# Performance work log

Hardware: AMD Instinct MI355X
Metric: run time of the kernel (lower is better)

The kernel has to match this reference:

```python
import jax, jax.numpy as jnp
import numpy as np

H = 16          # num heads
HD = 88         # head dim = 1408 / 16
IMG = 336
PATCH = 14
THETA = 10000.0
IDX = IMG // PATCH          # 24 patches per side
SEQ = IDX * IDX + 1         # 576 patches + 1 CLS slot = 577


def _vision_rope_cos_sin():
    # Faithful to HF Llama4VisionRotaryEmbedding (rope_type='llama4', complex64):
    # 2D rope over (x, y) patch coordinates; CLS token gets zero rotation.
    img_idx = np.arange(IDX * IDX, dtype=np.int64).reshape(-1, 1)
    img_idx = np.concatenate([img_idx, img_idx[:1]], axis=0)
    img_idx[-1, -1] = -2  # CLS token marker
    fx = img_idx % IDX
    fy = img_idx // IDX
    freq_dim = HD // 2  # 44
    rope_freq = 1.0 / (THETA ** (np.arange(0, freq_dim, 2)[: freq_dim // 2].astype(np.float64) / freq_dim))
    freqs_x = np.repeat((fx + 1)[..., None] * rope_freq[None, None, :], 2, axis=-1)
    freqs_y = np.repeat((fy + 1)[..., None] * rope_freq[None, None, :], 2, axis=-1)
    freqs = np.concatenate([freqs_x, freqs_y], axis=-1)[..., ::2]  # [SEQ, 1, HD//2]
    freqs = np.where(img_idx.reshape(-1, 1, 1) < 0, 0.0, freqs)
    return jnp.asarray(np.cos(freqs), jnp.float32), jnp.asarray(np.sin(freqs), jnp.float32)


def _apply_rope(x, cos, sin):
    # x: [B, S, H, HD]; treat last dim as HD//2 complex pairs, rotate by e^{i*freq}
    xr = x.reshape(*x.shape[:-1], HD // 2, 2)
    a, b = xr[..., 0], xr[..., 1]               # [B, S, H, HD//2]
    out_r = a * cos - b * sin                   # cos/sin [S,1,HD//2] broadcast over B,H
    out_i = a * sin + b * cos
    return jnp.stack([out_r, out_i], axis=-1).reshape(x.shape)


def setup_inputs() -> dict:
    key = jax.random.key(0)
    ks = jax.random.split(key, 9)
    D = H * HD  # 1408
    B, S = 32, SEQ
    s = 0.02
    return {
        "hidden_states": jax.random.normal(ks[0], (B, S, D), jnp.float32),
        "wq": jax.random.normal(ks[1], (D, D), jnp.float32) * s,
        "bq": jax.random.normal(ks[2], (D,), jnp.float32) * s,
        "wk": jax.random.normal(ks[3], (D, D), jnp.float32) * s,
        "bk": jax.random.normal(ks[4], (D,), jnp.float32) * s,
        "wv": jax.random.normal(ks[5], (D, D), jnp.float32) * s,
        "bv": jax.random.normal(ks[6], (D,), jnp.float32) * s,
        "wo": jax.random.normal(ks[7], (D, D), jnp.float32) * s,
        "bo": jax.random.normal(ks[8], (D,), jnp.float32) * s,
    }


def reference(hidden_states, wq, bq, wk, bk, wv, bv, wo, bo):
    B, S, D = hidden_states.shape
    cos, sin = _vision_rope_cos_sin()
    # QKV projections (torch Linear convention: y = x @ W.T + b)
    q = (hidden_states @ wq.T + bq).reshape(B, S, H, HD)
    k = (hidden_states @ wk.T + bk).reshape(B, S, H, HD)
    v = (hidden_states @ wv.T + bv).reshape(B, S, H, HD)
    q = _apply_rope(q, cos, sin)
    k = _apply_rope(k, cos, sin)
    # Full (non-causal) self-attention
    scores = jnp.einsum('bqhd,bkhd->bhqk', q, k) * (HD ** -0.5)
    probs = jax.nn.softmax(scores, axis=-1)
    attn = jnp.einsum('bhqk,bkhd->bqhd', probs, v).reshape(B, S, D)
    return attn @ wo.T + bo
```

## Files before the change

kernel.cpp:

```cpp
#include <hip/hip_runtime.h>
#include <hip/hip_bf16.h>
#include <cstdint>
#include <cstddef>

#define NHEADS 16
#define HDIM   88
#define SEQLEN 577
#define NBATCH 32
#define DMODEL 1408
#define MROWS  (NBATCH * SEQLEN)
#define MTILES 145
#define MPAD   (MTILES * 128)
#define SP     592
#define DP     96
#define NFREQ  44
#define NBH    (NBATCH * NHEADS)

typedef __attribute__((ext_vector_type(8))) short short8;
typedef __attribute__((ext_vector_type(4))) float floatx4;

__device__ __forceinline__ unsigned short f2bf(float f) {
    union { float f; unsigned u; } v; v.f = f;
    unsigned u = v.u;
    u += 0x7fffu + ((u >> 16) & 1u);
    return (unsigned short)(u >> 16);
}

__device__ __forceinline__ void gload_lds16(const void* g, void* lds) {
    __builtin_amdgcn_global_load_lds(
        (__attribute__((address_space(1))) unsigned int*)(void*)(g ? (void*)g : (void*)g),
        (__attribute__((address_space(3))) unsigned int*)lds, 16, 0, 0);
}

__global__ void l4v_rope_table(float* __restrict__ cos_t, float* __restrict__ sin_t) {
    int idx = blockIdx.x * blockDim.x + threadIdx.x;
    if (idx >= SEQLEN * NFREQ) return;
    int s = idx / NFREQ, j = idx % NFREQ;
    float ang = 0.0f;
    if (s != SEQLEN - 1) {
        int coord = (j < 22) ? (s % 24) : (s / 24);
        int i = (j < 22) ? j : j - 22;
        float rf = __expf(-(2.0f * (float)i / 44.0f) * 9.21034037197618f);
        ang = (float)(coord + 1) * rf;
    }
    cos_t[idx] = cosf(ang);
    sin_t[idx] = sinf(ang);
}

__global__ void l4v_cvt_bf16(const float* __restrict__ in, unsigned short* __restrict__ out, int n) {
    int i = (blockIdx.x * blockDim.x + threadIdx.x) * 4;
    if (i + 3 < n) {
        float4 f = *(const float4*)(in + i);
        ushort4 o;
        o.x = f2bf(f.x); o.y = f2bf(f.y); o.z = f2bf(f.z); o.w = f2bf(f.w);
        *(ushort4*)(out + i) = o;
    } else {
        for (; i < n; i++) out[i] = f2bf(in[i]);
    }
}

__global__ __launch_bounds__(256, 2)
void l4v_gemm128(const unsigned short* __restrict__ A,
                 const unsigned short* __restrict__ Bw,
                 const float* __restrict__ bias,
                 const float* __restrict__ cos_t,
                 const float* __restrict__ sin_t,
                 unsigned short* __restrict__ out_bf,
                 float* __restrict__ out_f32,
                 int mode)
{
    __shared__ __align__(16) unsigned short a_sm[128 * 32];
    __shared__ __align__(16) unsigned short b_sm[128 * 32];

    const int tid  = threadIdx.x;
    const int lane = tid & 63;
    const int w    = tid >> 6;
    const int quad = lane >> 4;
    const int c    = lane & 15;
    const int wr   = w >> 1;
    const int wc   = w & 1;
    const int m0   = blockIdx.y * 128;
    const int n0   = blockIdx.x * 128;

    floatx4 acc[4][4];
#pragma unroll
    for (int i = 0; i < 4; i++)
#pragma unroll
        for (int j = 0; j < 4; j++) acc[i][j] = (floatx4)0.0f;

    const int chunk0 = w * 128 + lane;
    const int chunk1 = w * 128 + 64 + lane;
    const int r0 = chunk0 >> 2, ch0 = chunk0 & 3;
    const int r1 = chunk1 >> 2, ch1 = chunk1 & 3;
    const unsigned short* Ab = A  + (size_t)m0 * DMODEL;
    const unsigned short* Bb = Bw + (size_t)n0 * DMODEL;

    for (int k0 = 0; k0 < DMODEL; k0 += 32) {
        gload_lds16(Ab + (size_t)r0 * DMODEL + k0 + ch0 * 8, a_sm + (w * 128) * 8);
        gload_lds16(Ab + (size_t)r1 * DMODEL + k0 + ch1 * 8, a_sm + (w * 128 + 64) * 8);
        gload_lds16(Bb + (size_t)r0 * DMODEL + k0 + ch0 * 8, b_sm + (w * 128) * 8);
        gload_lds16(Bb + (size_t)r1 * DMODEL + k0 + ch1 * 8, b_sm + (w * 128 + 64) * 8);
        __syncthreads();
        short8 af[4], bfr[4];
#pragma unroll
        for (int mt = 0; mt < 4; mt++)
            af[mt] = *(const short8*)(a_sm + (wr * 64 + mt * 16 + c) * 32 + quad * 8);
#pragma unroll
        for (int nt = 0; nt < 4; nt++)
            bfr[nt] = *(const short8*)(b_sm + (wc * 64 + nt * 16 + c) * 32 + quad * 8);
#pragma unroll
        for (int mt = 0; mt < 4; mt++)
#pragma unroll
            for (int nt = 0; nt < 4; nt++)
                acc[mt][nt] = __builtin_amdgcn_mfma_f32_16x16x32_bf16(af[mt], bfr[nt], acc[mt][nt], 0, 0, 0);
        __syncthreads();
    }

    if (mode == 3) {
#pragma unroll
        for (int mt = 0; mt < 4; mt++) {
            int mbase = m0 + wr * 64 + mt * 16 + quad * 4;
#pragma unroll
            for (int nt = 0; nt < 4; nt++) {
                int n = n0 + wc * 64 + nt * 16 + c;
                float bi = bias[n];
#pragma unroll
                for (int r = 0; r < 4; r++) {
                    int m = mbase + r;
                    if (m < MROWS) out_f32[(size_t)m * DMODEL + n] = acc[mt][nt][r] + bi;
                }
            }
        }
        return;
    }

    const bool rope = (mode < 2);
#pragma unroll
    for (int mt = 0; mt < 4; mt++) {
        int mbase = m0 + wr * 64 + mt * 16 + quad * 4;
#pragma unroll
        for (int nt = 0; nt < 4; nt++) {
            int n = n0 + wc * 64 + nt * 16 + c;
            float bi = bias[n];
            int h = n / HDIM, d = n % HDIM, j = d >> 1;
#pragma unroll
            for (int r = 0; r < 4; r++) {
                int m = mbase + r;
                int s = m % SEQLEN;
                int b = m / SEQLEN;
                float v = acc[mt][nt][r] + bi;
                float outv = v;
                if (rope) {
                    float pv = __shfl_xor(v, 1);
                    float cs = cos_t[s * NFREQ + j];
                    float sn = sin_t[s * NFREQ + j];
                    outv = ((d & 1) == 0) ? (v * cs - pv * sn) : (pv * sn + v * cs);
                }
                if (m < MROWS)
                    out_bf[((size_t)(b * NHEADS + h) * SP + s) * DP + d] = f2bf(outv);
            }
        }
    }
}

__global__ __launch_bounds__(256, 2)
void l4v_attn(const unsigned short* __restrict__ Q,
              const unsigned short* __restrict__ K,
              const unsigned short* __restrict__ V,
              unsigned short* __restrict__ Obuf)
{
    __shared__ __align__(16) unsigned short k_sm[64 * DP];
    __shared__ __align__(16) unsigned short v_sm[64 * DP];
    __shared__ __align__(16) unsigned short p_sm[4][16 * 64];

    const int tid  = threadIdx.x;
    const int lane = tid & 63;
    const int w    = tid >> 6;
    const int quad = lane >> 4;
    const int c    = lane & 15;
    const int qt   = blockIdx.x;
    const int bh   = blockIdx.y;
    const size_t base = (size_t)bh * SP * DP;

    short8 aq[3];
    {
        int qrow = qt * 64 + w * 16 + c;
        if (qrow > SP - 1) qrow = SP - 1;
#pragma unroll
        for (int ks = 0; ks < 3; ks++)
            aq[ks] = *(const short8*)(Q + base + (size_t)qrow * DP + ks * 32 + quad * 8);
    }

    float m_run[4], l_run[4];
    floatx4 o_acc[6];
#pragma unroll
    for (int r = 0; r < 4; r++) { m_run[r] = -INFINITY; l_run[r] = 0.0f; }
#pragma unroll
    for (int i = 0; i < 6; i++) o_acc[i] = (floatx4)0.0f;

    const float sl2e = 0.10660035817780522f * 1.4426950408889634f;

    for (int kt = 0; kt < 10; kt++) {
#pragma unroll
        for (int i = 0; i < 3; i++) {
            int chnk = w * 192 + i * 64 + lane;
            int row = chnk / 12, ch = chnk % 12;
            int krow = kt * 64 + row;
            if (krow > SP - 1) krow = SP - 1;
            gload_lds16(K + base + (size_t)krow * DP + ch * 8, k_sm + (w * 192 + i * 64) * 8);
            gload_lds16(V + base + (size_t)krow * DP + ch * 8, v_sm + (w * 192 + i * 64) * 8);
        }
        __syncthreads();

        floatx4 sc[4];
#pragma unroll
        for (int nt = 0; nt < 4; nt++) {
            sc[nt] = (floatx4)0.0f;
#pragma unroll
            for (int ks = 0; ks < 3; ks++) {
                short8 bk = *(const short8*)(k_sm + (nt * 16 + c) * DP + ks * 32 + quad * 8);
                sc[nt] = __builtin_amdgcn_mfma_f32_16x16x32_bf16(aq[ks], bk, sc[nt], 0, 0, 0);
            }
        }

        float t[4][4];
#pragma unroll
        for (int nt = 0; nt < 4; nt++) {
            int skcol = kt * 64 + nt * 16 + c;
            bool valid = (skcol < SEQLEN);
#pragma unroll
            for (int r = 0; r < 4; r++)
                t[nt][r] = valid ? sc[nt][r] * sl2e : -INFINITY;
        }

        float mnew[4], alpha[4];
#pragma unroll
        for (int r = 0; r < 4; r++) {
            float v = fmaxf(fmaxf(t[0][r], t[1][r]), fmaxf(t[2][r], t[3][r]));
#pragma unroll
            for (int off = 1; off < 16; off <<= 1) v = fmaxf(v, __shfl_xor(v, off));
            mnew[r] = fmaxf(m_run[r], v);
            alpha[r] = exp2f(m_run[r] - mnew[r]);
            m_run[r] = mnew[r];
        }

        float p[4][4];
#pragma unroll
        for (int nt = 0; nt < 4; nt++)
#pragma unroll
            for (int r = 0; r < 4; r++)
                p[nt][r] = exp2f(t[nt][r] - mnew[r]);

#pragma unroll
        for (int r = 0; r < 4; r++) {
            float sm = p[0][r] + p[1][r] + p[2][r] + p[3][r];
#pragma unroll
            for (int off = 1; off < 16; off <<= 1) sm += __shfl_xor(sm, off);
            l_run[r] = l_run[r] * alpha[r] + sm;
        }

#pragma unroll
        for (int nt = 0; nt < 4; nt++)
#pragma unroll
            for (int r = 0; r < 4; r++)
                p_sm[w][(quad * 4 + r) * 64 + nt * 16 + c] = f2bf(p[nt][r]);

#pragma unroll
        for (int i = 0; i < 6; i++)
#pragma unroll
            for (int r = 0; r < 4; r++)
                o_acc[i][r] *= alpha[r];

#pragma unroll
        for (int kp = 0; kp < 2; kp++) {
            short8 ap = *(const short8*)(&p_sm[w][c * 64 + kp * 32 + quad * 8]);
#pragma unroll
            for (int d2 = 0; d2 < 6; d2++) {
                short8 bv;
#pragma unroll
                for (int j = 0; j < 8; j++)
                    bv[j] = (short)v_sm[(kp * 32 + quad * 8 + j) * DP + d2 * 16 + c];
                o_acc[d2] = __builtin_amdgcn_mfma_f32_16x16x32_bf16(ap, bv, o_acc[d2], 0, 0, 0);
            }
        }
        __syncthreads();
    }

    const int b = bh >> 4, h = bh & 15;
#pragma unroll
    for (int r = 0; r < 4; r++) {
        int sq = qt * 64 + w * 16 + quad * 4 + r;
        float il = 1.0f / l_run[r];
        if (sq < SEQLEN) {
            size_t rowoff = ((size_t)b * SEQLEN + sq) * DMODEL + h * HDIM;
#pragma unroll
            for (int d2 = 0; d2 < 6; d2++) {
                int d = d2 * 16 + c;
                if (d < HDIM) Obuf[rowoff + d] = f2bf(o_acc[d2][r] * il);
            }
        }
    }
}

extern "C" void kernel_launch(void* const* d_in, const int* in_sizes, int n_in,
                              void* d_out, int out_size, void* d_ws, size_t ws_size,
                              hipStream_t stream)
{
    const float* hs = (const float*)d_in[0];
    const float* wq = (const float*)d_in[1];
    const float* bq = (const float*)d_in[2];
    const float* wk = (const float*)d_in[3];
    const float* bk = (const float*)d_in[4];
    const float* wv = (const float*)d_in[5];
    const float* bv = (const float*)d_in[6];
    const float* wo = (const float*)d_in[7];
    const float* bo = (const float*)d_in[8];
    float* out = (float*)d_out;

    char* ws = (char*)d_ws;
    size_t off = 0;
    auto alloc = [&](size_t bytes) -> char* {
        char* p = ws + off;
        off += (bytes + 255) & ~(size_t)255;
        return p;
    };

    unsigned short* hs_bf = (unsigned short*)alloc((size_t)MPAD * DMODEL * 2);
    unsigned short* wq_bf = (unsigned short*)alloc((size_t)DMODEL * DMODEL * 2);
    unsigned short* wk_bf = (unsigned short*)alloc((size_t)DMODEL * DMODEL * 2);
    unsigned short* wv_bf = (unsigned short*)alloc((size_t)DMODEL * DMODEL * 2);
    unsigned short* wo_bf = (unsigned short*)alloc((size_t)DMODEL * DMODEL * 2);
    unsigned short* qb    = (unsigned short*)alloc((size_t)NBH * SP * DP * 2);
    unsigned short* kb    = (unsigned short*)alloc((size_t)NBH * SP * DP * 2);
    unsigned short* vb    = (unsigned short*)alloc((size_t)NBH * SP * DP * 2);
    float* cos_t = (float*)alloc((size_t)SEQLEN * NFREQ * 4);
    float* sin_t = (float*)alloc((size_t)SEQLEN * NFREQ * 4);
    unsigned short* attn_bf = hs_bf;

    if (off > ws_size) return;

    l4v_rope_table<<<dim3((SEQLEN * NFREQ + 255) / 256), dim3(256), 0, stream>>>(cos_t, sin_t);

    const int nhs = MROWS * DMODEL;
    l4v_cvt_bf16<<<dim3(nhs / 4 / 256), dim3(256), 0, stream>>>(hs, hs_bf, nhs);
    const int nw = DMODEL * DMODEL;
    l4v_cvt_bf16<<<dim3(nw / 4 / 256), dim3(256), 0, stream>>>(wq, wq_bf, nw);
    l4v_cvt_bf16<<<dim3(nw / 4 / 256), dim3(256), 0, stream>>>(wk, wk_bf, nw);
    l4v_cvt_bf16<<<dim3(nw / 4 / 256), dim3(256), 0, stream>>>(wv, wv_bf, nw);
    l4v_cvt_bf16<<<dim3(nw / 4 / 256), dim3(256), 0, stream>>>(wo, wo_bf, nw);

    dim3 ggrid(DMODEL / 128, MTILES);
    l4v_gemm128<<<ggrid, dim3(256), 0, stream>>>(hs_bf, wq_bf, bq, cos_t, sin_t, qb, nullptr, 0);
    l4v_gemm128<<<ggrid, dim3(256), 0, stream>>>(hs_bf, wk_bf, bk, cos_t, sin_t, kb, nullptr, 1);
    l4v_gemm128<<<ggrid, dim3(256), 0, stream>>>(hs_bf, wv_bf, bv, cos_t, sin_t, vb, nullptr, 2);

    l4v_attn<<<dim3(10, NBH), dim3(256), 0, stream>>>(qb, kb, vb, attn_bf);

    l4v_gemm128<<<ggrid, dim3(256), 0, stream>>>(attn_bf, wo_bf, bo, cos_t, sin_t, nullptr, out, 3);
}
```

Before: 1.008 ms.

## Transpose V layout, fuse QKV GEMMs, pad attention LDS and batch query tiles

The GEMM epilogue now writes V in a transposed [bh, d, s] layout. The attention P·V step can then read V fragments with vector LDS loads instead of eight scalar gathers per fragment. The three QKV projections are merged into one launch that picks the weight by blockIdx, and the LDS strides for K, V and P are padded to cut bank conflicts. Each attention block now handles five query tiles with higher launch bounds. In exchange, the V stores in the GEMM become strided 2-byte scatters, K and V are staged through registers instead of direct-to-LDS loads, and the attention grid has fewer blocks.

```diff
diff --git a/kernel.cpp b/kernel.cpp
--- a/kernel.cpp
+++ b/kernel.cpp
@@ -12,6 +12,7 @@
 #define MTILES 145
 #define MPAD   (MTILES * 128)
 #define SP     592
+#define SPT    592
 #define DP     96
 #define NFREQ  44
 #define NBH    (NBATCH * NHEADS)
@@ -28,7 +29,7 @@
 
 __device__ __forceinline__ void gload_lds16(const void* g, void* lds) {
     __builtin_amdgcn_global_load_lds(
-        (__attribute__((address_space(1))) unsigned int*)(void*)(g ? (void*)g : (void*)g),
+        (__attribute__((address_space(1))) unsigned int*)g,
         (__attribute__((address_space(3))) unsigned int*)lds, 16, 0, 0);
 }
 
@@ -59,15 +60,125 @@
     }
 }
 
-__global__ __launch_bounds__(256, 2)
-void l4v_gemm128(const unsigned short* __restrict__ A,
-                 const unsigned short* __restrict__ Bw,
-                 const float* __restrict__ bias,
-                 const float* __restrict__ cos_t,
-                 const float* __restrict__ sin_t,
-                 unsigned short* __restrict__ out_bf,
-                 float* __restrict__ out_f32,
-                 int mode)
+__global__ __launch_bounds__(256, 3)
+void l4v_gemm_qkv(const unsigned short* __restrict__ A,
+                  const unsigned short* __restrict__ Wq,
+                  const unsigned short* __restrict__ Wk,
+                  const unsigned short* __restrict__ Wv,
+                  const float* __restrict__ Bq,
+                  const float* __restrict__ Bk,
+                  const float* __restrict__ Bv,
+                  const float* __restrict__ cos_t,
+                  const float* __restrict__ sin_t,
+                  unsigned short* __restrict__ Oq,
+                  unsigned short* __restrict__ Ok,
+                  unsigned short* __restrict__ OvT)
+{
+    __shared__ __align__(16) unsigned short a_sm[128 * 32];
+    __shared__ __align__(16) unsigned short b_sm[128 * 32];
+
+    const int tid  = threadIdx.x;
+    const int lane = tid & 63;
+    const int w    = tid >> 6;
+    const int quad = lane >> 4;
+    const int c    = lane & 15;
+    const int wr   = w >> 1;
+    const int wc   = w & 1;
+    const int sel  = blockIdx.x % 3;
+    const int n0   = (blockIdx.x / 3) * 128;
+    const int m0   = blockIdx.y * 128;
+
+    const unsigned short* Bw = (sel == 0) ? Wq : (sel == 1) ? Wk : Wv;
+    const float* bias        = (sel == 0) ? Bq : (sel == 1) ? Bk : Bv;
+
+    floatx4 acc[4][4];
+#pragma unroll
+    for (int i = 0; i < 4; i++)
+#pragma unroll
+        for (int j = 0; j < 4; j++) acc[i][j] = (floatx4)0.0f;
+
+    const int chunk0 = w * 128 + lane;
+    const int chunk1 = w * 128 + 64 + lane;
+    const int r0 = chunk0 >> 2, ch0 = chunk0 & 3;
+    const int r1 = chunk1 >> 2, ch1 = chunk1 & 3;
+    const unsigned short* Ab = A  + (size_t)m0 * DMODEL;
+    const unsigned short* Bb = Bw + (size_t)n0 * DMODEL;
+
+    for (int k0 = 0; k0 < DMODEL; k0 += 32) {
+        gload_lds16(Ab + (size_t)r0 * DMODEL + k0 + ch0 * 8, a_sm + (w * 128) * 8);
+        gload_lds16(Ab + (size_t)r1 * DMODEL + k0 + ch1 * 8, a_sm + (w * 128 + 64) * 8);
+        gload_lds16(Bb + (size_t)r0 * DMODEL + k0 + ch0 * 8, b_sm + (w * 128) * 8);
+        gload_lds16(Bb + (size_t)r1 * DMODEL + k0 + ch1 * 8, b_sm + (w * 128 + 64) * 8);
+        __syncthreads();
+        short8 af[4], bfr[4];
+#pragma unroll
+        for (int mt = 0; mt < 4; mt++)
+            af[mt] = *(const short8*)(a_sm + (wr * 64 + mt * 16 + c) * 32 + quad * 8);
+#pragma unroll
+        for (int nt = 0; nt < 4; nt++)
+            bfr[nt] = *(const short8*)(b_sm + (wc * 64 + nt * 16 + c) * 32 + quad * 8);
+#pragma unroll
+        for (int mt = 0; mt < 4; mt++)
+#pragma unroll
+            for (int nt = 0; nt < 4; nt++)
+                acc[mt][nt] = __builtin_amdgcn_mfma_f32_16x16x32_bf16(af[mt], bfr[nt], acc[mt][nt], 0, 0, 0);
+        __syncthreads();
+    }
+
+    if (sel < 2) {
+        unsigned short* outp = (sel == 0) ? Oq : Ok;
+#pragma unroll
+        for (int mt = 0; mt < 4; mt++) {
+            int mbase = m0 + wr * 64 + mt * 16 + quad * 4;
+#pragma unroll
+            for (int nt = 0; nt < 4; nt++) {
+                int n = n0 + wc * 64 + nt * 16 + c;
+                float bi = bias[n];
+                int h = n / HDIM, d = n % HDIM, j = d >> 1;
+#pragma unroll
+                for (int r = 0; r < 4; r++) {
+                    int m = mbase + r;
+                    int b = m / SEQLEN;
+                    int s = m - b * SEQLEN;
+                    float v = acc[mt][nt][r] + bi;
+                    float pv = __shfl_xor(v, 1);
+                    float cs = cos_t[s * NFREQ + j];
+                    float sn = sin_t[s * NFREQ + j];
+                    float outv = ((d & 1) == 0) ? (v * cs - pv * sn) : (pv * sn + v * cs);
+                    if (m < MROWS)
+                        outp[((size_t)(b * NHEADS + h) * SP + s) * DP + d] = f2bf(outv);
+                }
+            }
+        }
+    } else {
+#pragma unroll
+        for (int mt = 0; mt < 4; mt++) {
+            int mbase = m0 + wr * 64 + mt * 16 + quad * 4;
+#pragma unroll
+            for (int nt = 0; nt < 4; nt++) {
+                int n = n0 + wc * 64 + nt * 16 + c;
+                float bi = bias[n];
+                int h = n / HDIM, d = n % HDIM;
+#pragma unroll
+                for (int r = 0; r < 4; r++) {
+                    int m = mbase + r;
+                    if (m < MROWS) {
+                        int b = m / SEQLEN;
+                        int s = m - b * SEQLEN;
+                        OvT[((size_t)((b * NHEADS + h) * DP + d)) * SPT + s] =
+                            f2bf(acc[mt][nt][r] + bi);
+                    }
+                }
+            }
+        }
+    }
+}
+
+__global__ __launch_bounds__(256, 3)
+void l4v_gemm_out(const unsigned short* __restrict__ A,
+                  const unsigned short* __restrict__ Bw,
+                  const float* __restrict__ bias,
+                  float* __restrict__ out_f32)
 {
     __shared__ __align__(16) unsigned short a_sm[128 * 32];
     __shared__ __align__(16) unsigned short b_sm[128 * 32];
@@ -116,25 +227,6 @@
         __syncthreads();
     }
 
-    if (mode == 3) {
-#pragma unroll
-        for (int mt = 0; mt < 4; mt++) {
-            int mbase = m0 + wr * 64 + mt * 16 + quad * 4;
-#pragma unroll
-            for (int nt = 0; nt < 4; nt++) {
-                int n = n0 + wc * 64 + nt * 16 + c;
-                float bi = bias[n];
-#pragma unroll
-                for (int r = 0; r < 4; r++) {
-                    int m = mbase + r;
-                    if (m < MROWS) out_f32[(size_t)m * DMODEL + n] = acc[mt][nt][r] + bi;
-                }
-            }
-        }
-        return;
-    }
-
-    const bool rope = (mode < 2);
 #pragma unroll
     for (int mt = 0; mt < 4; mt++) {
         int mbase = m0 + wr * 64 + mt * 16 + quad * 4;
@@ -142,161 +234,153 @@
         for (int nt = 0; nt < 4; nt++) {
             int n = n0 + wc * 64 + nt * 16 + c;
             float bi = bias[n];
-            int h = n / HDIM, d = n % HDIM, j = d >> 1;
 #pragma unroll
             for (int r = 0; r < 4; r++) {
                 int m = mbase + r;
-                int s = m % SEQLEN;
-                int b = m / SEQLEN;
-                float v = acc[mt][nt][r] + bi;
-                float outv = v;
-                if (rope) {
-                    float pv = __shfl_xor(v, 1);
-                    float cs = cos_t[s * NFREQ + j];
-                    float sn = sin_t[s * NFREQ + j];
-                    outv = ((d & 1) == 0) ? (v * cs - pv * sn) : (pv * sn + v * cs);
-                }
-                if (m < MROWS)
-                    out_bf[((size_t)(b * NHEADS + h) * SP + s) * DP + d] = f2bf(outv);
+                if (m < MROWS) out_f32[(size_t)m * DMODEL + n] = acc[mt][nt][r] + bi;
             }
         }
     }
 }
 
-__global__ __launch_bounds__(256, 2)
+__global__ __launch_bounds__(256, 4)
 void l4v_attn(const unsigned short* __restrict__ Q,
               const unsigned short* __restrict__ K,
-              const unsigned short* __restrict__ V,
+              const unsigned short* __restrict__ VT,
               unsigned short* __restrict__ Obuf)
 {
-    __shared__ __align__(16) unsigned short k_sm[64 * DP];
-    __shared__ __align__(16) unsigned short v_sm[64 * DP];
-    __shared__ __align__(16) unsigned short p_sm[4][16 * 64];
+    __shared__ __align__(16) unsigned short k_sm[64 * 104];
+    __shared__ __align__(16) unsigned short v_sm[96 * 72];
+    __shared__ __align__(16) unsigned short p_sm[4][16 * 72];
 
     const int tid  = threadIdx.x;
     const int lane = tid & 63;
     const int w    = tid >> 6;
     const int quad = lane >> 4;
     const int c    = lane & 15;
-    const int qt   = blockIdx.x;
     const int bh   = blockIdx.y;
-    const size_t base = (size_t)bh * SP * DP;
-
-    short8 aq[3];
-    {
+    const int b    = bh >> 4, h = bh & 15;
+    const size_t base  = (size_t)bh * SP * DP;
+    const size_t baseT = (size_t)bh * DP * SPT;
+    const float sl2e = 0.10660035817780522f * 1.4426950408889634f;
+
+    for (int qi = 0; qi < 5; qi++) {
+        const int qt = blockIdx.x * 5 + qi;
+
         int qrow = qt * 64 + w * 16 + c;
         if (qrow > SP - 1) qrow = SP - 1;
+        short8 aq[3];
 #pragma unroll
         for (int ks = 0; ks < 3; ks++)
             aq[ks] = *(const short8*)(Q + base + (size_t)qrow * DP + ks * 32 + quad * 8);
-    }
-
-    float m_run[4], l_run[4];
-    floatx4 o_acc[6];
-#pragma unroll
-    for (int r = 0; r < 4; r++) { m_run[r] = -INFINITY; l_run[r] = 0.0f; }
-#pragma unroll
-    for (int i = 0; i < 6; i++) o_acc[i] = (floatx4)0.0f;
-
-    const float sl2e = 0.10660035817780522f * 1.4426950408889634f;
-
-    for (int kt = 0; kt < 10; kt++) {
-#pragma unroll
-        for (int i = 0; i < 3; i++) {
-            int chnk = w * 192 + i * 64 + lane;
-            int row = chnk / 12, ch = chnk % 12;
-            int krow = kt * 64 + row;
-            if (krow > SP - 1) krow = SP - 1;
-            gload_lds16(K + base + (size_t)krow * DP + ch * 8, k_sm + (w * 192 + i * 64) * 8);
-            gload_lds16(V + base + (size_t)krow * DP + ch * 8, v_sm + (w * 192 + i * 64) * 8);
+
+        float m_run[4], l_run[4];
+        floatx4 o_acc[6];
+#pragma unroll
+        for (int r = 0; r < 4; r++) { m_run[r] = -INFINITY; l_run[r] = 0.0f; }
+#pragma unroll
+        for (int i = 0; i < 6; i++) o_acc[i] = (floatx4)0.0f;
+
+        for (int kt = 0; kt < 10; kt++) {
+#pragma unroll
+            for (int i = 0; i < 3; i++) {
+                int cc = tid + i * 256;
+                int krr = cc / 12, kcol = cc - krr * 12;
+                int krow = kt * 64 + krr;
+                if (krow > SP - 1) krow = SP - 1;
+                float4 kd = *(const float4*)(K + base + (size_t)krow * DP + kcol * 8);
+                *(float4*)(k_sm + krr * 104 + kcol * 8) = kd;
+
+                int vrow = cc >> 3, vcol = cc & 7;
+                int scol = kt * 64 + vcol * 8;
+                if (scol > SPT - 8) scol = SPT - 8;
+                float4 vd = *(const float4*)(VT + baseT + (size_t)vrow * SPT + scol);
+                *(float4*)(v_sm + vrow * 72 + vcol * 8) = vd;
+            }
+            __syncthreads();
+
+            floatx4 sc[4];
+#pragma unroll
+            for (int nt = 0; nt < 4; nt++) {
+                sc[nt] = (floatx4)0.0f;
+#pragma unroll
+                for (int ks = 0; ks < 3; ks++) {
+                    short8 bk = *(const short8*)(k_sm + (nt * 16 + c) * 104 + ks * 32 + quad * 8);
+                    sc[nt] = __builtin_amdgcn_mfma_f32_16x16x32_bf16(aq[ks], bk, sc[nt], 0, 0, 0);
+                }
+            }
+
+            float t[4][4];
+#pragma unroll
+            for (int nt = 0; nt < 4; nt++) {
+                int skcol = kt * 64 + nt * 16 + c;
+                bool valid = (skcol < SEQLEN);
+#pragma unroll
+                for (int r = 0; r < 4; r++)
+                    t[nt][r] = valid ? sc[nt][r] * sl2e : -INFINITY;
+            }
+
+            float mnew[4], alpha[4];
+#pragma unroll
+            for (int r = 0; r < 4; r++) {
+                float v = fmaxf(fmaxf(t[0][r], t[1][r]), fmaxf(t[2][r], t[3][r]));
+#pragma unroll
+                for (int off = 1; off < 16; off <<= 1) v = fmaxf(v, __shfl_xor(v, off));
+                mnew[r] = fmaxf(m_run[r], v);
+                alpha[r] = exp2f(m_run[r] - mnew[r]);
+                m_run[r] = mnew[r];
+            }
+
+            float p[4][4];
+#pragma unroll
+            for (int nt = 0; nt < 4; nt++)
+#pragma unroll
+                for (int r = 0; r < 4; r++)
+                    p[nt][r] = exp2f(t[nt][r] - mnew[r]);
+
+#pragma unroll
+            for (int r = 0; r < 4; r++) {
+                float sm = p[0][r] + p[1][r] + p[2][r] + p[3][r];
+#pragma unroll
+                for (int off = 1; off < 16; off <<= 1) sm += __shfl_xor(sm, off);
+                l_run[r] = l_run[r] * alpha[r] + sm;
+            }
+
+#pragma unroll
+            for (int nt = 0; nt < 4; nt++)
+#pragma unroll
+                for (int r = 0; r < 4; r++)
+                    p_sm[w][(quad * 4 + r) * 72 + nt * 16 + c] = f2bf(p[nt][r]);
+
+#pragma unroll
+            for (int i = 0; i < 6; i++)
+#pragma unroll
+                for (int r = 0; r < 4; r++)
+                    o_acc[i][r] *= alpha[r];
+
+#pragma unroll
+            for (int kp = 0; kp < 2; kp++) {
+                short8 ap = *(const short8*)(&p_sm[w][c * 72 + kp * 32 + quad * 8]);
+#pragma unroll
+                for (int d2 = 0; d2 < 6; d2++) {
+                    short8 bv = *(const short8*)(v_sm + (d2 * 16 + c) * 72 + kp * 32 + quad * 8);
+                    o_acc[d2] = __builtin_amdgcn_mfma_f32_16x16x32_bf16(ap, bv, o_acc[d2], 0, 0, 0);
+                }
+            }
+            __syncthreads();
         }
-        __syncthreads();
-
-        floatx4 sc[4];
-#pragma unroll
-        for (int nt = 0; nt < 4; nt++) {
-            sc[nt] = (floatx4)0.0f;
-#pragma unroll
-            for (int ks = 0; ks < 3; ks++) {
-                short8 bk = *(const short8*)(k_sm + (nt * 16 + c) * DP + ks * 32 + quad * 8);
-                sc[nt] = __builtin_amdgcn_mfma_f32_16x16x32_bf16(aq[ks], bk, sc[nt], 0, 0, 0);
-            }
-        }
-
-        float t[4][4];
-#pragma unroll
-        for (int nt = 0; nt < 4; nt++) {
-            int skcol = kt * 64 + nt * 16 + c;
-            bool valid = (skcol < SEQLEN);
-#pragma unroll
-            for (int r = 0; r < 4; r++)
-                t[nt][r] = valid ? sc[nt][r] * sl2e : -INFINITY;
-        }
-
-        float mnew[4], alpha[4];
+
 #pragma unroll
         for (int r = 0; r < 4; r++) {
-            float v = fmaxf(fmaxf(t[0][r], t[1][r]), fmaxf(t[2][r], t[3][r]));
-#pragma unroll
-            for (int off = 1; off < 16; off <<= 1) v = fmaxf(v, __shfl_xor(v, off));
-            mnew[r] = fmaxf(m_run[r], v);
-            alpha[r] = exp2f(m_run[r] - mnew[r]);
-            m_run[r] = mnew[r];
-        }
-
-        float p[4][4];
-#pragma unroll
-        for (int nt = 0; nt < 4; nt++)
-#pragma unroll
-            for (int r = 0; r < 4; r++)
-                p[nt][r] = exp2f(t[nt][r] - mnew[r]);
-
-#pragma unroll
-        for (int r = 0; r < 4; r++) {
-            float sm = p[0][r] + p[1][r] + p[2][r] + p[3][r];
-#pragma unroll
-            for (int off = 1; off < 16; off <<= 1) sm += __shfl_xor(sm, off);
-            l_run[r] = l_run[r] * alpha[r] + sm;
-        }
-
-#pragma unroll
-        for (int nt = 0; nt < 4; nt++)
-#pragma unroll
-            for (int r = 0; r < 4; r++)
-                p_sm[w][(quad * 4 + r) * 64 + nt * 16 + c] = f2bf(p[nt][r]);
-
-#pragma unroll
-        for (int i = 0; i < 6; i++)
-#pragma unroll
-            for (int r = 0; r < 4; r++)
-                o_acc[i][r] *= alpha[r];
-
-#pragma unroll
-        for (int kp = 0; kp < 2; kp++) {
-            short8 ap = *(const short8*)(&p_sm[w][c * 64 + kp * 32 + quad * 8]);
-#pragma unroll
-            for (int d2 = 0; d2 < 6; d2++) {
-                short8 bv;
-#pragma unroll
-                for (int j = 0; j < 8; j++)
-                    bv[j] = (short)v_sm[(kp * 32 + quad * 8 + j) * DP + d2 * 16 + c];
-                o_acc[d2] = __builtin_amdgcn_mfma_f32_16x16x32_bf16(ap, bv, o_acc[d2], 0, 0, 0);
-            }
-        }
-        __syncthreads();
-    }
-
-    const int b = bh >> 4, h = bh & 15;
-#pragma unroll
-    for (int r = 0; r < 4; r++) {
-        int sq = qt * 64 + w * 16 + quad * 4 + r;
-        float il = 1.0f / l_run[r];
-        if (sq < SEQLEN) {
-            size_t rowoff = ((size_t)b * SEQLEN + sq) * DMODEL + h * HDIM;
-#pragma unroll
-            for (int d2 = 0; d2 < 6; d2++) {
-                int d = d2 * 16 + c;
-                if (d < HDIM) Obuf[rowoff + d] = f2bf(o_acc[d2][r] * il);
+            int sq = qt * 64 + w * 16 + quad * 4 + r;
+            float il = 1.0f / l_run[r];
+            if (sq < SEQLEN) {
+                size_t rowoff = ((size_t)b * SEQLEN + sq) * DMODEL + h * HDIM;
+#pragma unroll
+                for (int d2 = 0; d2 < 6; d2++) {
+                    int d = d2 * 16 + c;
+                    if (d < HDIM) Obuf[rowoff + d] = f2bf(o_acc[d2][r] * il);
+                }
             }
         }
     }
@@ -332,7 +416,7 @@
     unsigned short* wo_bf = (unsigned short*)alloc((size_t)DMODEL * DMODEL * 2);
     unsigned short* qb    = (unsigned short*)alloc((size_t)NBH * SP * DP * 2);
     unsigned short* kb    = (unsigned short*)alloc((size_t)NBH * SP * DP * 2);
-    unsigned short* vb    = (unsigned short*)alloc((size_t)NBH * SP * DP * 2);
+    unsigned short* vt    = (unsigned short*)alloc((size_t)NBH * DP * SPT * 2);
     float* cos_t = (float*)alloc((size_t)SEQLEN * NFREQ * 4);
     float* sin_t = (float*)alloc((size_t)SEQLEN * NFREQ * 4);
     unsigned short* attn_bf = hs_bf;
@@ -349,12 +433,10 @@
     l4v_cvt_bf16<<<dim3(nw / 4 / 256), dim3(256), 0, stream>>>(wv, wv_bf, nw);
     l4v_cvt_bf16<<<dim3(nw / 4 / 256), dim3(256), 0, stream>>>(wo, wo_bf, nw);
 
-    dim3 ggrid(DMODEL / 128, MTILES);
-    l4v_gemm128<<<ggrid, dim3(256), 0, stream>>>(hs_bf, wq_bf, bq, cos_t, sin_t, qb, nullptr, 0);
-    l4v_gemm128<<<ggrid, dim3(256), 0, stream>>>(hs_bf, wk_bf, bk, cos_t, sin_t, kb, nullptr, 1);
-    l4v_gemm128<<<ggrid, dim3(256), 0, stream>>>(hs_bf, wv_bf, bv, cos_t, sin_t, vb, nullptr, 2);
-
-    l4v_attn<<<dim3(10, NBH), dim3(256), 0, stream>>>(qb, kb, vb, attn_bf);
-
-    l4v_gemm128<<<ggrid, dim3(256), 0, stream>>>(attn_bf, wo_bf, bo, cos_t, sin_t, nullptr, out, 3);
-}
+    l4v_gemm_qkv<<<dim3(33, MTILES), dim3(256), 0, stream>>>(
+        hs_bf, wq_bf, wk_bf, wv_bf, bq, bk, bv, cos_t, sin_t, qb, kb, vt);
+
+    l4v_attn<<<dim3(2, NBH), dim3(256), 0, stream>>>(qb, kb, vt, attn_bf);
+
+    l4v_gemm_out<<<dim3(DMODEL / 128, MTILES), dim3(256), 0, stream>>>(attn_bf, wo_bf, bo, out);
+}
```

Result: slower. 1.043 ms (+3.5%).
